# Kernel optimization log

Hardware: AMD Instinct MI355X
Metric: run time of the kernel (lower is better)

## Reference

```python
import jax, jax.numpy as jnp
import numpy as np

D_MODEL = 1024
N_HEADS = 16
DIM_HEAD = D_MODEL // N_HEADS
SCALE = DIM_HEAD ** -0.5


def setup_inputs() -> dict:
    key = jax.random.key(0)
    ks = jax.random.split(key, 7)
    B, N = 2, 2048
    q = jax.random.normal(ks[0], (B, N, D_MODEL), dtype=jnp.float32)
    # boolean mask: True = masked out; keep sparse so softmax rows stay valid
    mask = jax.random.bernoulli(ks[1], 0.1, (B, N, N))
    s = D_MODEL ** -0.5
    Wq = jax.random.normal(ks[2], (D_MODEL, D_MODEL), dtype=jnp.float32) * s
    Wk = jax.random.normal(ks[3], (D_MODEL, D_MODEL), dtype=jnp.float32) * s
    Wv = jax.random.normal(ks[4], (D_MODEL, D_MODEL), dtype=jnp.float32) * s
    Wo = jax.random.normal(ks[5], (D_MODEL, D_MODEL), dtype=jnp.float32) * s
    bo = jnp.zeros((D_MODEL,), dtype=jnp.float32)
    return {"q": q, "mask": mask, "Wq": Wq, "Wk": Wk, "Wv": Wv, "Wo": Wo, "bo": bo}


def reference(q, mask, Wq, Wk, Wv, Wo, bo):
    B, N, D = q.shape
    # self-attention: memory = q. nn.Linear applies x @ W.T (W is [out, in]).
    qh = (q @ Wq.T) * SCALE
    kh = q @ Wk.T
    vh = q @ Wv.T
    # b n (h d) -> b h n d
    qh = qh.reshape(B, N, N_HEADS, DIM_HEAD).transpose(0, 2, 1, 3)
    kh = kh.reshape(B, N, N_HEADS, DIM_HEAD).transpose(0, 2, 1, 3)
    vh = vh.reshape(B, N, N_HEADS, DIM_HEAD).transpose(0, 2, 1, 3)
    scores = jnp.einsum('bhid,bhjd->bhij', qh, kh)  # [B,H,N,N]
    mask_value = -jnp.finfo(scores.dtype).max
    scores = jnp.where(mask[:, None, :, :], mask_value, scores)
    attn = jax.nn.softmax(scores, axis=-1)
    o = jnp.einsum('bhij,bhjd->bhid', attn, vh)
    o = o.transpose(0, 2, 1, 3).reshape(B, N, D)  # b h n d -> b n (h d)
    return o @ Wo.T + bo
```

## Files before the change

### kernel.cpp

```cpp
#include <hip/hip_runtime.h>
#include <hip/hip_bf16.h>

typedef float fx4  __attribute__((ext_vector_type(4)));
typedef float fx16 __attribute__((ext_vector_type(16)));
typedef short s16x8 __attribute__((ext_vector_type(8)));

#define NSEQ 2048
#define DM   1024
#define NH   16
#define DH   64
#define MROWS 4096
#define NWORDS (2 * NSEQ * (NSEQ / 64))

#define QK_SCALE (0.125f * 1.44269504088896f)

__device__ __forceinline__ unsigned short f2bf(float f) {
    union { float f; unsigned u; } c; c.f = f;
    unsigned u = c.u;
    unsigned r = u + 0x7FFFu + ((u >> 16) & 1u);
    return (unsigned short)(r >> 16);
}

__device__ __forceinline__ float exp2_fast(float x) {
#if __has_builtin(__builtin_amdgcn_exp2f)
    return __builtin_amdgcn_exp2f(x);
#else
    return exp2f(x);
#endif
}

__device__ __forceinline__ unsigned cvt_pk_bf16(float a, float b) {
    unsigned r;
    asm("v_cvt_pk_bf16_f32 %0, %1, %2" : "=v"(r) : "v"(a), "v"(b));
    return r;
}

__device__ __forceinline__ fx4 zero4() {
    fx4 z; z[0] = 0.f; z[1] = 0.f; z[2] = 0.f; z[3] = 0.f; return z;
}

__device__ __forceinline__ fx16 zero16() {
    fx16 z;
#pragma unroll
    for (int i = 0; i < 16; i++) z[i] = 0.f;
    return z;
}

__device__ __forceinline__ void gload16(const void* g, void* l) {
    __builtin_amdgcn_global_load_lds(
        (const __attribute__((address_space(1))) unsigned int*)g,
        (__attribute__((address_space(3))) unsigned int*)l,
        16, 0, 0);
}

__global__ void cvt_kernel(const float* __restrict__ in,
                           unsigned short* __restrict__ out, int n4) {
    int i = blockIdx.x * blockDim.x + threadIdx.x;
    if (i >= n4) return;
    float4 v = reinterpret_cast<const float4*>(in)[i];
    ushort4 o;
    o.x = f2bf(v.x); o.y = f2bf(v.y); o.z = f2bf(v.z); o.w = f2bf(v.w);
    reinterpret_cast<ushort4*>(out)[i] = o;
}

__global__ void cvt4_kernel(const float* __restrict__ w0, const float* __restrict__ w1,
                            const float* __restrict__ w2, const float* __restrict__ w3,
                            unsigned short* __restrict__ o0, unsigned short* __restrict__ o1,
                            unsigned short* __restrict__ o2, unsigned short* __restrict__ o3) {
    const float* in; unsigned short* out;
    switch (blockIdx.y) {
        case 0:  in = w0; out = o0; break;
        case 1:  in = w1; out = o1; break;
        case 2:  in = w2; out = o2; break;
        default: in = w3; out = o3; break;
    }
    int i = blockIdx.x * blockDim.x + threadIdx.x;
    float4 v = reinterpret_cast<const float4*>(in)[i];
    ushort4 o;
    o.x = f2bf(v.x); o.y = f2bf(v.y); o.z = f2bf(v.z); o.w = f2bf(v.w);
    reinterpret_cast<ushort4*>(out)[i] = o;
}

__global__ void mask_detect(const unsigned int* __restrict__ m, int* __restrict__ flag) {
    unsigned mx = 0;
    int stride = gridDim.x * blockDim.x;
    for (int i = blockIdx.x * blockDim.x + threadIdx.x; i < (2 * NSEQ * NSEQ) / 4; i += stride) {
        unsigned v = m[i];
        mx = v > mx ? v : mx;
    }
    if (__any(mx > 1u)) {
        if ((threadIdx.x & 63) == 0) atomicOr(flag, 1);
    }
}

__global__ void mask_pack(const void* __restrict__ mask, const int* __restrict__ mflag,
                          unsigned long long* __restrict__ packed) {
    const int flg  = mflag[0];
    const int lane = threadIdx.x & 63;
    const int wpb  = blockDim.x >> 6;
    const int perm = (lane & 3) + 8 * ((lane >> 2) & 3) + 4 * (lane >> 5) + 32 * ((lane >> 4) & 1);
    size_t w = (size_t)blockIdx.x * wpb + (threadIdx.x >> 6);
    const size_t stride = (size_t)gridDim.x * wpb;
    for (; w < NWORDS; w += stride) {
        size_t elem = (w >> 5) * (size_t)NSEQ + (size_t)(w & 31) * 64 + perm;
        int mv = flg ? (int)((const unsigned char*)mask)[elem]
                     : ((const int*)mask)[elem];
        unsigned long long bits = __ballot(mv != 0);
        if (lane == 0) packed[w] = bits;
    }
}

__global__ __launch_bounds__(256) void gemm_qkv(
        const unsigned short* __restrict__ A,
        const unsigned short* __restrict__ Wq,
        const unsigned short* __restrict__ Wk,
        const unsigned short* __restrict__ Wv,
        unsigned short* __restrict__ Qh,
        unsigned short* __restrict__ Kh,
        unsigned short* __restrict__ VhT) {
    __shared__ unsigned short As[128 * 32];
    __shared__ unsigned short Bs[128 * 32];

    const int tid  = threadIdx.x;
    const int lane = tid & 63;
    const int w    = tid >> 6;
    const int lr   = lane & 15;
    const int lg   = lane >> 4;
    const int wr   = (w >> 1) * 64;
    const int wc   = (w & 1) * 64;
    const int rowbase = blockIdx.y * 128;
    const int seg     = blockIdx.x >> 3;
    const int cb      = (blockIdx.x & 7) * 128;
    const unsigned short* W = seg == 0 ? Wq : (seg == 1 ? Wk : Wv);
    const float scale = seg == 0 ? QK_SCALE : 1.0f;

    fx4 acc[4][4];
#pragma unroll
    for (int i = 0; i < 4; i++)
#pragma unroll
        for (int j = 0; j < 4; j++) acc[i][j] = zero4();

    for (int k0 = 0; k0 < DM; k0 += 32) {
        __syncthreads();
#pragma unroll
        for (int i = 0; i < 2; i++) {
            int j = i * 256 + w * 64 + lane;
            int r = j >> 2, c8 = (j & 3) * 8;
            gload16(A + (size_t)(rowbase + r) * DM + k0 + c8,
                    As + (size_t)(i * 256 + w * 64) * 8);
            gload16(W + (size_t)(cb + r) * DM + k0 + c8,
                    Bs + (size_t)(i * 256 + w * 64) * 8);
        }
        __syncthreads();

        s16x8 af[4], bf[4];
#pragma unroll
        for (int mi = 0; mi < 4; mi++)
            af[mi] = *reinterpret_cast<const s16x8*>(&As[(wr + mi * 16 + lr) * 32 + 8 * lg]);
#pragma unroll
        for (int ni = 0; ni < 4; ni++)
            bf[ni] = *reinterpret_cast<const s16x8*>(&Bs[(wc + ni * 16 + lr) * 32 + 8 * lg]);
#pragma unroll
        for (int mi = 0; mi < 4; mi++)
#pragma unroll
            for (int ni = 0; ni < 4; ni++)
                acc[mi][ni] = __builtin_amdgcn_mfma_f32_16x16x32_bf16(af[mi], bf[ni], acc[mi][ni], 0, 0, 0);
    }

#pragma unroll
    for (int mi = 0; mi < 4; mi++) {
#pragma unroll
        for (int ni = 0; ni < 4; ni++) {
#pragma unroll
            for (int v = 0; v < 4; v++) {
                int m    = rowbase + wr + mi * 16 + lg * 4 + v;
                int cseg = cb + wc + ni * 16 + lr;
                float val = acc[mi][ni][v] * scale;
                int b = m >> 11, nseq = m & 2047;
                int h = cseg >> 6, dh = cseg & 63;
                if (seg < 2) {
                    unsigned short* dst = seg == 0 ? Qh : Kh;
                    dst[((size_t)(b * NH + h) * NSEQ + nseq) * DH + dh] = f2bf(val);
                } else {
                    VhT[((size_t)(b * NH + h) * DH + dh) * NSEQ + nseq] = f2bf(val);
                }
            }
        }
    }
}

__global__ __launch_bounds__(256) void gemm_out(
        const unsigned short* __restrict__ A,
        const unsigned short* __restrict__ W,
        float* __restrict__ out,
        const float* __restrict__ bias) {
    __shared__ unsigned short As[64 * 32];
    __shared__ unsigned short Bs[128 * 32];

    const int tid  = threadIdx.x;
    const int lane = tid & 63;
    const int w    = tid >> 6;
    const int lr   = lane & 15;
    const int lg   = lane >> 4;
    const int wr   = (w >> 1) * 32;
    const int wc   = (w & 1) * 64;
    const int rowbase = blockIdx.y * 64;
    const int colbase = blockIdx.x * 128;

    fx4 acc[2][4];
#pragma unroll
    for (int i = 0; i < 2; i++)
#pragma unroll
        for (int j = 0; j < 4; j++) acc[i][j] = zero4();

    for (int k0 = 0; k0 < DM; k0 += 32) {
        __syncthreads();
        {
            int j = tid;
            int r = j >> 2, c8 = (j & 3) * 8;
            gload16(A + (size_t)(rowbase + r) * DM + k0 + c8,
                    As + (size_t)(w * 64) * 8);
            gload16(W + (size_t)(colbase + r) * DM + k0 + c8,
                    Bs + (size_t)(w * 64) * 8);
            int r2 = 64 + (j >> 2);
            gload16(W + (size_t)(colbase + r2) * DM + k0 + c8,
                    Bs + (size_t)(256 + w * 64) * 8);
        }
        __syncthreads();

        s16x8 af[2], bf[4];
#pragma unroll
        for (int mi = 0; mi < 2; mi++)
            af[mi] = *reinterpret_cast<const s16x8*>(&As[(wr + mi * 16 + lr) * 32 + 8 * lg]);
#pragma unroll
        for (int ni = 0; ni < 4; ni++)
            bf[ni] = *reinterpret_cast<const s16x8*>(&Bs[(wc + ni * 16 + lr) * 32 + 8 * lg]);
#pragma unroll
        for (int mi = 0; mi < 2; mi++)
#pragma unroll
            for (int ni = 0; ni < 4; ni++)
                acc[mi][ni] = __builtin_amdgcn_mfma_f32_16x16x32_bf16(af[mi], bf[ni], acc[mi][ni], 0, 0, 0);
    }

#pragma unroll
    for (int mi = 0; mi < 2; mi++)
#pragma unroll
        for (int ni = 0; ni < 4; ni++)
#pragma unroll
            for (int v = 0; v < 4; v++) {
                int m = rowbase + wr + mi * 16 + lg * 4 + v;
                int c = colbase + wc + ni * 16 + lr;
                out[(size_t)m * DM + c] = acc[mi][ni][v] + bias[c];
            }
}

__global__ __launch_bounds__(256) void attn_kernel(
        const unsigned short* __restrict__ Qh,
        const unsigned short* __restrict__ Kh,
        const unsigned short* __restrict__ VhT,
        const unsigned long long* __restrict__ Mp,
        unsigned short* __restrict__ Obuf) {
    __shared__ unsigned short Ks[2][64 * 64];
    __shared__ unsigned short Vs[2][64 * 64];

    const int tid  = threadIdx.x;
    const int lane = tid & 63;
    const int w    = tid >> 6;
    const int l31  = lane & 31;
    const int hi   = lane >> 5;

    const int wg    = ((blockIdx.x & 7) << 6) | (blockIdx.x >> 3);
    const int qbase = (wg & 15) << 7;
    const int bh    = wg >> 4;
    const int b     = bh >> 4;
    const int h     = bh & 15;

    s16x8 qf[4];
    const size_t qrow = (size_t)bh * NSEQ + qbase + w * 32 + l31;
#pragma unroll
    for (int s = 0; s < 4; s++)
        qf[s] = *reinterpret_cast<const s16x8*>(Qh + qrow * DH + s * 16 + hi * 8);

    float mreg = -3.0e38f, lrow = 0.f;
    fx16 po[2];
    po[0] = zero16(); po[1] = zero16();

    const size_t mbase = ((size_t)b * NSEQ + qbase + w * 32 + l31) * (NSEQ / 64);

    auto stage = [&](int d, int kv0) {
#pragma unroll
        for (int i = 0; i < 2; i++) {
            int u  = i * 256 + w * 64 + lane;
            int r  = u >> 3, cs = u & 7;
            int cu = cs ^ (r & 7);
            gload16(Kh + ((size_t)bh * NSEQ + kv0 + r) * DH + cu * 8,
                    &Ks[d][(size_t)(i * 256 + w * 64) * 8]);
            gload16(VhT + ((size_t)bh * DH + r) * NSEQ + kv0 + cu * 8,
                    &Vs[d][(size_t)(i * 256 + w * 64) * 8]);
        }
    };

    stage(0, 0);
    __syncthreads();

    for (int it = 0; it < NSEQ / 64; it++) {
        const int cur = it & 1;
        if (it < NSEQ / 64 - 1) stage(cur ^ 1, (it + 1) << 6);

        unsigned long long pwm = Mp[mbase + it];
        unsigned m32 = (unsigned)(pwm >> (hi * 32));

        fx16 sx[2];
        __builtin_amdgcn_s_setprio(1);
#pragma unroll
        for (int kh = 0; kh < 2; kh++) {
            sx[kh] = zero16();
            int r = kh * 32 + l31;
#pragma unroll
            for (int s = 0; s < 4; s++) {
                int cs = (2 * s + hi) ^ (r & 7);
                s16x8 kf = *reinterpret_cast<const s16x8*>(&Ks[cur][r * 64 + cs * 8]);
                sx[kh] = __builtin_amdgcn_mfma_f32_32x32x16_bf16(kf, qf[s], sx[kh], 0, 0, 0);
            }
        }
        __builtin_amdgcn_s_setprio(0);

        float tmax = -3.0e38f;
#pragma unroll
        for (int kh = 0; kh < 2; kh++)
#pragma unroll
            for (int reg = 0; reg < 16; reg++) {
                float sv = (m32 & (1u << (kh * 16 + reg))) ? -3.0e38f : sx[kh][reg];
                sx[kh][reg] = sv;
                tmax = fmaxf(tmax, sv);
            }
        tmax = fmaxf(tmax, __shfl_xor(tmax, 32));

        if (__any(tmax > mreg + 8.0f)) {
            float mn = fmaxf(mreg, tmax);
            float sc = exp2_fast(mreg - mn);
            mreg = mn;
            lrow *= sc;
#pragma unroll
            for (int reg = 0; reg < 16; reg++) {
                int qr = (reg & 3) + 8 * (reg >> 2) + 4 * hi;
                float scq = __shfl(sc, qr);
                po[0][reg] *= scq;
                po[1][reg] *= scq;
            }
        }

        float psum = 0.f;
#pragma unroll
        for (int kh = 0; kh < 2; kh++)
#pragma unroll
            for (int reg = 0; reg < 16; reg++) {
                float p = exp2_fast(sx[kh][reg] - mreg);
                sx[kh][reg] = p;
                psum += p;
            }
        psum += __shfl_xor(psum, 32);
        lrow += psum;

        __builtin_amdgcn_s_setprio(1);
#pragma unroll
        for (int ks = 0; ks < 4; ks++) {
            const int kh = ks >> 1, rb = (ks & 1) * 8;
            unsigned o0w0 = cvt_pk_bf16(sx[kh][rb + 0], sx[kh][rb + 1]);
            unsigned o0w1 = cvt_pk_bf16(sx[kh][rb + 2], sx[kh][rb + 3]);
            unsigned o1w0 = cvt_pk_bf16(sx[kh][rb + 4], sx[kh][rb + 5]);
            unsigned o1w1 = cvt_pk_bf16(sx[kh][rb + 6], sx[kh][rb + 7]);
            asm("v_permlane32_swap_b32 %0, %1" : "+v"(o0w0), "+v"(o1w0));
            asm("v_permlane32_swap_b32 %0, %1" : "+v"(o0w1), "+v"(o1w1));
            union { unsigned u[4]; s16x8 v; } pk;
            pk.u[0] = o0w0; pk.u[1] = o0w1; pk.u[2] = o1w0; pk.u[3] = o1w1;
#pragma unroll
            for (int dt = 0; dt < 2; dt++) {
                int r  = dt * 32 + l31;
                int cs = (2 * ks + hi) ^ (r & 7);
                s16x8 vf = *reinterpret_cast<const s16x8*>(&Vs[cur][r * 64 + cs * 8]);
                po[dt] = __builtin_amdgcn_mfma_f32_32x32x16_bf16(pk.v, vf, po[dt], 0, 0, 0);
            }
        }
        __builtin_amdgcn_s_setprio(0);

        __syncthreads();
    }

    float inv = 1.0f / lrow;
#pragma unroll
    for (int reg = 0; reg < 16; reg++) {
        int qr = (reg & 3) + 8 * (reg >> 2) + 4 * hi;
        float invq = __shfl(inv, qr);
        int q = qbase + w * 32 + qr;
#pragma unroll
        for (int dt = 0; dt < 2; dt++) {
            int d = dt * 32 + l31;
            Obuf[((size_t)b * NSEQ + q) * DM + h * DH + d] = f2bf(po[dt][reg] * invq);
        }
    }
}

extern "C" void kernel_launch(void* const* d_in, const int* in_sizes, int n_in,
                              void* d_out, int out_size, void* d_ws, size_t ws_size,
                              hipStream_t stream) {
    const float* q    = (const float*)d_in[0];
    const void*  mask = (const void*)d_in[1];
    const float* Wq   = (const float*)d_in[2];
    const float* Wk   = (const float*)d_in[3];
    const float* Wv   = (const float*)d_in[4];
    const float* Wo   = (const float*)d_in[5];
    const float* bo   = (const float*)d_in[6];
    float* out = (float*)d_out;

    char* ws = (char*)d_ws;
    const size_t MB = 1024 * 1024;
    unsigned short* qbf  = (unsigned short*)(ws + 0);
    unsigned long long* packed = (unsigned long long*)(ws + 0);
    unsigned short* Wqb  = (unsigned short*)(ws + 8  * MB);
    unsigned short* Wkb  = (unsigned short*)(ws + 10 * MB);
    unsigned short* Wvb  = (unsigned short*)(ws + 12 * MB);
    unsigned short* Wob  = (unsigned short*)(ws + 14 * MB);
    unsigned short* Qh   = (unsigned short*)(ws + 16 * MB);
    unsigned short* Kh   = (unsigned short*)(ws + 24 * MB);
    unsigned short* VhT  = (unsigned short*)(ws + 32 * MB);
    unsigned short* Obuf = (unsigned short*)(ws + 40 * MB);
    int*            flag = (int*)(ws + 56 * MB);

    hipMemsetAsync(flag, 0, 4, stream);
    mask_detect<<<1024, 256, 0, stream>>>((const unsigned int*)mask, flag);

    cvt_kernel<<<4096, 256, 0, stream>>>(q, qbf, (2 * NSEQ * DM) / 4);
    cvt4_kernel<<<dim3(1024, 4), 256, 0, stream>>>(Wq, Wk, Wv, Wo, Wqb, Wkb, Wvb, Wob);

    gemm_qkv<<<dim3(24, 32), 256, 0, stream>>>(qbf, Wqb, Wkb, Wvb, Qh, Kh, VhT);

    mask_pack<<<1024, 256, 0, stream>>>(mask, flag, packed);

    attn_kernel<<<512, 256, 0, stream>>>(Qh, Kh, VhT, packed, Obuf);

    gemm_out<<<dim3(8, 64), 256, 0, stream>>>(Obuf, Wob, out, bo);
}
```

Baseline: 253.9 us.

## Split attention KV range across two wave groups and merge partial softmax

Doubles the attention block to 512 threads. Each half of the block processes half of the key/value sequence for the same query tile, with its own double-buffered LDS tiles. At the end the partial outputs, row maxima and row sums are exchanged through LDS and merged flash-decoding style. The aim is more waves per CU so MFMA work and loads overlap better, given only 512 blocks exist. The cost is doubled LDS use, an extra merge step, and the second group sitting idle during the final write.

Measured after the change: 256.6 us. Within noise of the previous version (+1.1%).

```diff
diff --git a/kernel.cpp b/kernel.cpp
--- a/kernel.cpp
+++ b/kernel.cpp
@@ -254,18 +254,21 @@
             }
 }
 
-__global__ __launch_bounds__(256) void attn_kernel(
+__global__ __launch_bounds__(512) void attn_kernel(
         const unsigned short* __restrict__ Qh,
         const unsigned short* __restrict__ Kh,
         const unsigned short* __restrict__ VhT,
         const unsigned long long* __restrict__ Mp,
         unsigned short* __restrict__ Obuf) {
-    __shared__ unsigned short Ks[2][64 * 64];
-    __shared__ unsigned short Vs[2][64 * 64];
+    __shared__ unsigned short Ks[2][2][64 * 64];
+    __shared__ unsigned short Vs[2][2][64 * 64];
 
     const int tid  = threadIdx.x;
     const int lane = tid & 63;
-    const int w    = tid >> 6;
+    const int w8   = tid >> 6;
+    const int grp  = w8 >> 2;
+    const int w    = w8 & 3;
+    const int gt   = tid & 255;
     const int l31  = lane & 31;
     const int hi   = lane >> 5;
 
@@ -290,24 +293,25 @@
     auto stage = [&](int d, int kv0) {
 #pragma unroll
         for (int i = 0; i < 2; i++) {
-            int u  = i * 256 + w * 64 + lane;
+            int u  = i * 256 + gt;
             int r  = u >> 3, cs = u & 7;
             int cu = cs ^ (r & 7);
             gload16(Kh + ((size_t)bh * NSEQ + kv0 + r) * DH + cu * 8,
-                    &Ks[d][(size_t)(i * 256 + w * 64) * 8]);
+                    &Ks[grp][d][(size_t)(i * 256 + w * 64) * 8]);
             gload16(VhT + ((size_t)bh * DH + r) * NSEQ + kv0 + cu * 8,
-                    &Vs[d][(size_t)(i * 256 + w * 64) * 8]);
+                    &Vs[grp][d][(size_t)(i * 256 + w * 64) * 8]);
         }
     };
 
-    stage(0, 0);
+    const int kvbase = grp << 10;
+    stage(0, kvbase);
     __syncthreads();
 
-    for (int it = 0; it < NSEQ / 64; it++) {
+    for (int it = 0; it < 16; it++) {
         const int cur = it & 1;
-        if (it < NSEQ / 64 - 1) stage(cur ^ 1, (it + 1) << 6);
-
-        unsigned long long pwm = Mp[mbase + it];
+        if (it < 15) stage(cur ^ 1, kvbase + ((it + 1) << 6));
+
+        unsigned long long pwm = Mp[mbase + grp * 16 + it];
         unsigned m32 = (unsigned)(pwm >> (hi * 32));
 
         fx16 sx[2];
@@ -319,7 +323,7 @@
 #pragma unroll
             for (int s = 0; s < 4; s++) {
                 int cs = (2 * s + hi) ^ (r & 7);
-                s16x8 kf = *reinterpret_cast<const s16x8*>(&Ks[cur][r * 64 + cs * 8]);
+                s16x8 kf = *reinterpret_cast<const s16x8*>(&Ks[grp][cur][r * 64 + cs * 8]);
                 sx[kh] = __builtin_amdgcn_mfma_f32_32x32x16_bf16(kf, qf[s], sx[kh], 0, 0, 0);
             }
         }
@@ -378,7 +382,7 @@
             for (int dt = 0; dt < 2; dt++) {
                 int r  = dt * 32 + l31;
                 int cs = (2 * ks + hi) ^ (r & 7);
-                s16x8 vf = *reinterpret_cast<const s16x8*>(&Vs[cur][r * 64 + cs * 8]);
+                s16x8 vf = *reinterpret_cast<const s16x8*>(&Vs[grp][cur][r * 64 + cs * 8]);
                 po[dt] = __builtin_amdgcn_mfma_f32_32x32x16_bf16(pk.v, vf, po[dt], 0, 0, 0);
             }
         }
@@ -387,16 +391,45 @@
         __syncthreads();
     }
 
-    float inv = 1.0f / lrow;
-#pragma unroll
-    for (int reg = 0; reg < 16; reg++) {
-        int qr = (reg & 3) + 8 * (reg >> 2) + 4 * hi;
-        float invq = __shfl(inv, qr);
-        int q = qbase + w * 32 + qr;
-#pragma unroll
-        for (int dt = 0; dt < 2; dt++) {
-            int d = dt * 32 + l31;
-            Obuf[((size_t)b * NSEQ + q) * DM + h * DH + d] = f2bf(po[dt][reg] * invq);
+    float* exPo = (float*)Ks;
+    float* exML = (float*)Vs;
+    if (grp == 1) {
+#pragma unroll
+        for (int dt = 0; dt < 2; dt++)
+#pragma unroll
+            for (int reg = 0; reg < 16; reg++)
+                exPo[w * 64 + lane + (dt * 16 + reg) * 256] = po[dt][reg];
+        exML[w * 64 + lane] = mreg;
+        exML[1024 + w * 64 + lane] = lrow;
+    }
+    __syncthreads();
+    if (grp == 0) {
+        float mB = exML[w * 64 + lane];
+        float lB = exML[1024 + w * 64 + lane];
+        float M  = fmaxf(mreg, mB);
+        float sA = exp2_fast(mreg - M);
+        float sB = exp2_fast(mB - M);
+        lrow = sA * lrow + sB * lB;
+#pragma unroll
+        for (int reg = 0; reg < 16; reg++) {
+            int qr = (reg & 3) + 8 * (reg >> 2) + 4 * hi;
+            float sAq = __shfl(sA, qr);
+            float sBq = __shfl(sB, qr);
+            po[0][reg] = sAq * po[0][reg] + sBq * exPo[w * 64 + lane + reg * 256];
+            po[1][reg] = sAq * po[1][reg] + sBq * exPo[w * 64 + lane + (16 + reg) * 256];
+        }
+
+        float inv = 1.0f / lrow;
+#pragma unroll
+        for (int reg = 0; reg < 16; reg++) {
+            int qr = (reg & 3) + 8 * (reg >> 2) + 4 * hi;
+            float invq = __shfl(inv, qr);
+            int q = qbase + w * 32 + qr;
+#pragma unroll
+            for (int dt = 0; dt < 2; dt++) {
+                int d = dt * 32 + l31;
+                Obuf[((size_t)b * NSEQ + q) * DM + h * DH + d] = f2bf(po[dt][reg] * invq);
+            }
         }
     }
 }
@@ -437,7 +470,7 @@
 
     mask_pack<<<1024, 256, 0, stream>>>(mask, flag, packed);
 
-    attn_kernel<<<512, 256, 0, stream>>>(Qh, Kh, VhT, packed, Obuf);
+    attn_kernel<<<512, 512, 0, stream>>>(Qh, Kh, VhT, packed, Obuf);
 
     gemm_out<<<dim3(8, 64), 256, 0, stream>>>(Obuf, Wob, out, bo);
 }
```
